# Optimization experiments

Hardware: AMD Instinct MI355X
Metric: run time of the kernel (lower is better)

The kernel has to match this reference:

```python
import math
import jax, jax.numpy as jnp
import numpy as np

NUM_EMBED = 2048
EMBED_FEATS = 64
IN_FEATS = 512
B, T = 16, 4096
COMMITMENT_COST = 0.25


def setup_inputs() -> dict:
    key = jax.random.key(0)
    k1, k2, k3, k4 = jax.random.split(key, 4)
    x = jax.random.normal(k1, (B, IN_FEATS, T), dtype=jnp.float32)
    proj_w = jax.random.normal(k2, (EMBED_FEATS, IN_FEATS), dtype=jnp.float32) / np.sqrt(IN_FEATS)
    proj_b = jax.random.normal(k3, (EMBED_FEATS,), dtype=jnp.float32) * 0.01
    embed = jax.random.normal(k4, (NUM_EMBED, EMBED_FEATS), dtype=jnp.float32)
    return {"x": x, "proj_w": proj_w, "proj_b": proj_b, "embed": embed}


def reference(x, proj_w, proj_b, embed):
    # 1x1 Conv1d projection, then transpose(1,-1): [B, Cin, T] -> [B, T, E]
    h = jnp.einsum('ec,bct->bte', proj_w, x) + proj_b  # [B, T, E]
    Bb, Tt, E = h.shape
    K = embed.shape[0]
    flat = h.reshape(-1, E)  # [N, E]
    # squared distances to codewords: [N, K]
    d2 = (jnp.sum(flat * flat, axis=1, keepdims=True)
          + jnp.sum(embed * embed, axis=1)
          - 2.0 * flat @ embed.T)
    q_idx = jnp.argmin(d2, axis=1)  # [N]
    z_q = embed[q_idx].reshape(Bb, Tt, E)  # one-hot @ embed == gather
    # commitment loss (codebook updated by EMA, so only commitment term)
    commitment = jnp.mean((jax.lax.stop_gradient(z_q) - h) ** 2)
    loss = COMMITMENT_COST * commitment
    # straight-through estimator
    z_q_st = h + jax.lax.stop_gradient(z_q - h)
    # code usage stats
    N = flat.shape[0]
    probs = jnp.zeros((K,), dtype=jnp.float32).at[q_idx].add(1.0) / N
    log_perplexity = -jnp.sum(probs * jnp.log(probs + 1e-10))
    kldiv_r = math.log(K) * (N / Bb) * jnp.ones((Bb, 1), dtype=jnp.float32)
    z_q_out = jnp.swapaxes(z_q_st, 1, 2)  # [B, E, T]
    return z_q_out, loss, kldiv_r, log_perplexity
```

## Files before the change

kernel.cpp:

```cpp
#include <hip/hip_runtime.h>
#include <math.h>

#define B_ 16
#define T_ 4096
#define C_ 512
#define E_ 64
#define K_ 2048
#define N_ (B_*T_)
#define ZQ_ELEMS 4194304

typedef __attribute__((ext_vector_type(8))) short short8;
typedef __attribute__((ext_vector_type(4))) short short4v;
typedef __attribute__((ext_vector_type(4))) float f32x4;

#define WS_EHI   0
#define WS_ELO   262144
#define WS_NHCC  524288
#define WS_WHI   532480
#define WS_WLO   598016
#define WS_HIST  663552
#define WS_LOSS  671744
#define WS_HIMG  1048576
#define WS_NEED  (WS_HIMG + 512*16384*2)

struct HiLo { short hi, lo; };

__device__ __forceinline__ unsigned short rne16(float v) {
    unsigned u = __float_as_uint(v);
    return (unsigned short)((u + 0x7FFFu + ((u >> 16) & 1u)) >> 16);
}
__device__ __forceinline__ HiLo split_rne(float v) {
    HiLo r;
    unsigned hb = rne16(v);
    r.hi = (short)hb;
    float hf = __uint_as_float((unsigned)hb << 16);
    r.lo = (short)rne16(v - hf);
    return r;
}

typedef const __attribute__((address_space(1))) void* gas1_t;
typedef __attribute__((address_space(3))) void* las3_t;
__device__ __forceinline__ void gl16(const void* g, void* l) {
    __builtin_amdgcn_global_load_lds((gas1_t)g, (las3_t)l, 16, 0, 0);
}

__global__ void prep_kernel(const float* __restrict__ embed,
                            const float* __restrict__ W,
                            short* __restrict__ ehi, short* __restrict__ elo,
                            float* __restrict__ nhcc,
                            short* __restrict__ whi, short* __restrict__ wlo) {
    const int tid = threadIdx.x;
    if (blockIdx.x < 64) {
        const int row = blockIdx.x * 32 + (tid >> 3);
        const int g = tid & 7;
        const float* src = embed + (size_t)row * 64 + g * 8;
        short8 hv, lv;
        float s = 0.f;
#pragma unroll
        for (int j = 0; j < 8; ++j) {
            float v = src[j];
            s = fmaf(v, v, s);
            HiLo r = split_rne(v);
            hv[j] = r.hi; lv[j] = r.lo;
        }
        const int c128 = row >> 7, r = row & 127;
        const int kt = r >> 4, col = r & 15, ks = g >> 2, qe = g & 3;
        const int slot = (kt * 2 + ks) * 64 + qe * 16 + col;
        *(short8*)(ehi + c128 * 8192 + slot * 8) = hv;
        *(short8*)(elo + c128 * 8192 + slot * 8) = lv;
        s += __shfl_xor(s, 1, 64);
        s += __shfl_xor(s, 2, 64);
        s += __shfl_xor(s, 4, 64);
        if (g == 0) nhcc[row] = -0.5f * s;
    } else {
        int idx = ((blockIdx.x - 64) * 256 + tid) * 4;
        float4 v = *(const float4*)(W + idx);
        short4v h, l;
        HiLo a = split_rne(v.x); h[0] = a.hi; l[0] = a.lo;
        HiLo b = split_rne(v.y); h[1] = b.hi; l[1] = b.lo;
        HiLo c = split_rne(v.z); h[2] = c.hi; l[2] = c.lo;
        HiLo d = split_rne(v.w); h[3] = d.hi; l[3] = d.lo;
        *(short4v*)(whi + idx) = h;
        *(short4v*)(wlo + idx) = l;
    }
}

__global__ __launch_bounds__(256, 2) void proj_kernel(
        const float* __restrict__ x,
        const short* __restrict__ whi, const short* __restrict__ wlo,
        const float* __restrict__ bias,
        short* __restrict__ himg, float* __restrict__ lossacc) {
    __shared__ __align__(16) float xw[4 * 32 * 66];

    const int tid = threadIdx.x;
    const int wave = tid >> 6, lane = tid & 63;
    const int row16 = lane & 15, quad = lane >> 4;
    const int blk = blockIdx.x;
    const int b  = blk >> 4;
    const int t0 = (blk & 15) * 256;
    const int t0w = t0 + wave * 64;
    const float* xr = x + (size_t)b * C_ * T_ + t0w;
    float* wl = xw + wave * (32 * 66);

    const int c_row = lane >> 4;
    const int c_t4  = (lane & 15) * 4;

    f32x4 acc[4][4];
#pragma unroll
    for (int rt = 0; rt < 4; ++rt)
#pragma unroll
        for (int et = 0; et < 4; ++et) acc[rt][et] = (f32x4){0.f, 0.f, 0.f, 0.f};

    float4 xn[8];
#pragma unroll
    for (int q = 0; q < 8; ++q)
        xn[q] = *(const float4*)(xr + (size_t)(q * 4 + c_row) * T_ + c_t4);

    for (int it = 0; it < 16; ++it) {
        const int c0 = it * 32;
#pragma unroll
        for (int q = 0; q < 8; ++q) {
            float* d = wl + (q * 4 + c_row) * 66 + c_t4;
            *(float2*)(d)     = make_float2(xn[q].x, xn[q].y);
            *(float2*)(d + 2) = make_float2(xn[q].z, xn[q].w);
        }
        if (it < 15) {
#pragma unroll
            for (int q = 0; q < 8; ++q)
                xn[q] = *(const float4*)(xr + (size_t)(c0 + 32 + q * 4 + c_row) * T_ + c_t4);
        }
#pragma unroll
        for (int rp = 0; rp < 2; ++rp) {
            short8 bh[2], bl[2];
#pragma unroll
            for (int rr = 0; rr < 2; ++rr) {
                const int rt = rp * 2 + rr;
#pragma unroll
                for (int j = 0; j < 8; ++j) {
                    float v = wl[(quad * 8 + j) * 66 + rt * 16 + row16];
                    HiLo r = split_rne(v);
                    bh[rr][j] = r.hi; bl[rr][j] = r.lo;
                }
            }
#pragma unroll
            for (int et = 0; et < 4; ++et) {
                size_t aoff = (size_t)(et * 16 + row16) * C_ + c0 + quad * 8;
                short8 ah = *(const short8*)(whi + aoff);
                short8 al = *(const short8*)(wlo + aoff);
#pragma unroll
                for (int rr = 0; rr < 2; ++rr) {
                    const int rt = rp * 2 + rr;
                    acc[rt][et] = __builtin_amdgcn_mfma_f32_16x16x32_bf16(ah, bh[rr], acc[rt][et], 0, 0, 0);
                    acc[rt][et] = __builtin_amdgcn_mfma_f32_16x16x32_bf16(al, bh[rr], acc[rt][et], 0, 0, 0);
                    acc[rt][et] = __builtin_amdgcn_mfma_f32_16x16x32_bf16(ah, bl[rr], acc[rt][et], 0, 0, 0);
                    acc[rt][et] = __builtin_amdgcn_mfma_f32_16x16x32_bf16(al, bl[rr], acc[rt][et], 0, 0, 0);
                }
            }
        }
    }

    float hh = 0.f;
#pragma unroll
    for (int rt = 0; rt < 4; ++rt) {
        const int tile16 = wave * 4 + rt;
        short* gb = himg + (size_t)(blk * 2 + (tile16 >> 3)) * 16384;
        const int w2 = tile16 & 7;
#pragma unroll
        for (int et = 0; et < 4; ++et) {
            float4 bv = *(const float4*)(bias + et * 16 + quad * 4);
            f32x4 a = acc[rt][et];
            a[0] += bv.x; a[1] += bv.y; a[2] += bv.z; a[3] += bv.w;
            hh = fmaf(a[0], a[0], hh); hh = fmaf(a[1], a[1], hh);
            hh = fmaf(a[2], a[2], hh); hh = fmaf(a[3], a[3], hh);
            short4v hv, lv;
#pragma unroll
            for (int r = 0; r < 4; ++r) {
                HiLo sp = split_rne(a[r]);
                hv[r] = sp.hi; lv[r] = sp.lo;
            }
            const int ks = et >> 1;
            const int qe = (et & 1) * 2 + (quad >> 1);
            const int j0 = (quad & 1) * 4;
            const int sl = ((w2 * 2 + ks) * 64 + qe * 16 + row16) * 8 + j0;
            *(short4v*)(gb + sl) = hv;
            *(short4v*)(gb + 8192 + sl) = lv;
        }
    }
#pragma unroll
    for (int m = 1; m < 64; m <<= 1) hh += __shfl_xor(hh, m, 64);
    if (lane == 0) atomicAdd(lossacc, hh);
}

#define VQ_STEP(H0, H1, L0, L1, SS)                                            \
    {                                                                          \
        const int kk = ((SS) >> 2) * 128 + (kh * 4 + ((SS) & 3)) * 16 + row16; \
        const float ci = nhcc[kk];                                             \
        _Pragma("unroll")                                                      \
        for (int rt = 0; rt < 4; ++rt) {                                       \
            f32x4 a2 = (f32x4){0.f, 0.f, 0.f, 0.f};                            \
            a2 = __builtin_amdgcn_mfma_f32_16x16x32_bf16(a_hi[rt][0], H0, a2, 0, 0, 0); \
            a2 = __builtin_amdgcn_mfma_f32_16x16x32_bf16(a_hi[rt][1], H1, a2, 0, 0, 0); \
            a2 = __builtin_amdgcn_mfma_f32_16x16x32_bf16(a_lo[rt][0], H0, a2, 0, 0, 0); \
            a2 = __builtin_amdgcn_mfma_f32_16x16x32_bf16(a_lo[rt][1], H1, a2, 0, 0, 0); \
            a2 = __builtin_amdgcn_mfma_f32_16x16x32_bf16(a_hi[rt][0], L0, a2, 0, 0, 0); \
            a2 = __builtin_amdgcn_mfma_f32_16x16x32_bf16(a_hi[rt][1], L1, a2, 0, 0, 0); \
            _Pragma("unroll")                                                  \
            for (int rg = 0; rg < 4; ++rg) {                                   \
                float v = a2[rg] + ci;                                         \
                if (v > vmax[rt][rg]) { vmax[rt][rg] = v; vidx[rt][rg] = kk; } \
            }                                                                  \
        }                                                                      \
    }

#define VQ_LOAD(H0, H1, L0, L1, SS)                                            \
    {                                                                          \
        const int c2 = (SS) >> 2, kt2 = kh * 4 + ((SS) & 3);                   \
        const short* pb = ehi + c2 * 8192 + kt2 * 1024;                        \
        const short* pl = elo + c2 * 8192 + kt2 * 1024;                        \
        H0 = *(const short8*)(pb + lane * 8);                                  \
        H1 = *(const short8*)(pb + 512 + lane * 8);                            \
        L0 = *(const short8*)(pl + lane * 8);                                  \
        L1 = *(const short8*)(pl + 512 + lane * 8);                            \
    }

__global__ __launch_bounds__(256, 2) void vq_kernel(
        const short* __restrict__ himg,
        const short* __restrict__ ehi, const short* __restrict__ elo,
        const float* __restrict__ nhcc,
        const float* __restrict__ embed, float* __restrict__ out,
        int* __restrict__ hist, float* __restrict__ lossacc) {
    __shared__ __align__(16) float tile[128 * 69];
    __shared__ int   qsm[128];
    __shared__ float vtmp[128];
    __shared__ int   itmp[128];

    const int tid = threadIdx.x;
    const int wave = tid >> 6, lane = tid & 63;
    const int row16 = lane & 15, quad = lane >> 4;
    const int g = blockIdx.x;
    const int b  = g >> 5;
    const int t0 = (g & 31) * 128;
    const int rowgrp = wave & 1, kh = wave >> 1;

    const short* gb = himg + (size_t)g * 16384;
    short8 a_hi[4][2], a_lo[4][2];
#pragma unroll
    for (int rt = 0; rt < 4; ++rt)
#pragma unroll
        for (int ks = 0; ks < 2; ++ks) {
            const int w2 = rowgrp * 4 + rt;
            const int sl = ((w2 * 2 + ks) * 64 + lane) * 8;
            a_hi[rt][ks] = *(const short8*)(gb + sl);
            a_lo[rt][ks] = *(const short8*)(gb + 8192 + sl);
        }

    float vmax[4][4];
    int   vidx[4][4];
#pragma unroll
    for (int rt = 0; rt < 4; ++rt)
#pragma unroll
        for (int rg = 0; rg < 4; ++rg) { vmax[rt][rg] = -3.4e38f; vidx[rt][rg] = 0; }

    short8 pAh0, pAh1, pAl0, pAl1;
    short8 pBh0, pBh1, pBl0, pBl1;
    VQ_LOAD(pAh0, pAh1, pAl0, pAl1, 0);
    for (int s = 0; s < 64; s += 2) {
        VQ_LOAD(pBh0, pBh1, pBl0, pBl1, s + 1);
        VQ_STEP(pAh0, pAh1, pAl0, pAl1, s);
        if (s + 2 < 64) VQ_LOAD(pAh0, pAh1, pAl0, pAl1, s + 2);
        VQ_STEP(pBh0, pBh1, pBl0, pBl1, s + 1);
    }

    float s_loss = 0.f;
#pragma unroll
    for (int rt = 0; rt < 4; ++rt)
#pragma unroll
        for (int rg = 0; rg < 4; ++rg) {
            float v = vmax[rt][rg];
            int ix = vidx[rt][rg];
#pragma unroll
            for (int m = 1; m < 16; m <<= 1) {
                float ov = __shfl_xor(v, m, 64);
                int   oi = __shfl_xor(ix, m, 64);
                if (ov > v || (ov == v && oi < ix)) { v = ov; ix = oi; }
            }
            vmax[rt][rg] = v; vidx[rt][rg] = ix;
        }
    if (kh == 1 && row16 == 0) {
#pragma unroll
        for (int rt = 0; rt < 4; ++rt)
#pragma unroll
            for (int rg = 0; rg < 4; ++rg) {
                const int row = (rowgrp * 4 + rt) * 16 + quad * 4 + rg;
                vtmp[row] = vmax[rt][rg];
                itmp[row] = vidx[rt][rg];
            }
    }
    __syncthreads();
    if (kh == 0) {
        if (row16 == 0) {
#pragma unroll
            for (int rt = 0; rt < 4; ++rt)
#pragma unroll
                for (int rg = 0; rg < 4; ++rg) {
                    const int row = (rowgrp * 4 + rt) * 16 + quad * 4 + rg;
                    float v = vmax[rt][rg];
                    int ix = vidx[rt][rg];
                    const float ov = vtmp[row];
                    const int   oi = itmp[row];
                    if (ov > v || (ov == v && oi < ix)) { v = ov; ix = oi; }
                    qsm[row] = ix;
                    atomicAdd(&hist[ix], 1);
                    s_loss += v;
                }
        }
        s_loss += __shfl_xor(s_loss, 16, 64);
        s_loss += __shfl_xor(s_loss, 32, 64);
        if (lane == 0) atomicAdd(lossacc, -2.f * s_loss);
    }
    __syncthreads();

    {
        const int r = tid >> 1, piece = tid & 1;
        const float* src = embed + (size_t)qsm[r] * 64 + piece * 32;
        float* dst = tile + r * 69 + piece * 32;
#pragma unroll
        for (int j = 0; j < 8; ++j)
            *(float4*)(dst + j * 4) = *(const float4*)(src + j * 4);
    }
    __syncthreads();
    {
        const int tt = tid & 63;
        const int eo = tid >> 6;
        float* ob = out + ((size_t)b * 64) * T_ + t0;
#pragma unroll
        for (int j = 0; j < 16; ++j) {
            const int e = j * 4 + eo;
            ob[(size_t)e * T_ + tt]      = tile[tt * 69 + e];
            ob[(size_t)e * T_ + 64 + tt] = tile[(tt + 64) * 69 + e];
        }
    }
}

__global__ __launch_bounds__(512, 4) void projvq_kernel(
        const float* __restrict__ x,
        const short* __restrict__ whi, const short* __restrict__ wlo,
        const float* __restrict__ bias,
        const short* __restrict__ ehi, const short* __restrict__ elo,
        const float* __restrict__ nhcc,
        const float* __restrict__ embed, float* __restrict__ out,
        int* __restrict__ hist, float* __restrict__ lossacc) {
    __shared__ __align__(16) char smem[68096];
    float* xsf  = (float*)smem;
    short* es   = (short*)smem;
    short* aimg = (short*)(smem + 32768);
    float* ccs  = (float*)(smem + 65536);
    int*   qsm2 = (int*)(smem + 66560);
    float* vtmp = (float*)(smem + 67072);
    int*   itmp = (int*)(smem + 67584);
    float* tile = (float*)smem;

    const int tid = threadIdx.x;
    const int wave = tid >> 6, lane = tid & 63;
    const int row16 = lane & 15, quad = lane >> 4;
    const int b  = blockIdx.x >> 5;
    const int t0 = (blockIdx.x & 31) * 128;
    const float* xb = x + (size_t)b * C_ * T_ + t0;

    f32x4 cc = *(const f32x4*)(nhcc + tid * 4);

    f32x4 acc[4];
#pragma unroll
    for (int et = 0; et < 4; ++et) acc[et] = (f32x4){0.f, 0.f, 0.f, 0.f};

#pragma unroll
    for (int j = 0; j < 2; ++j) {
        int o = j * 512 + tid;
        gl16(xb + (size_t)(o >> 5) * T_ + (o & 31) * 4, xsf + o * 4);
    }
    __syncthreads();

    for (int it = 0; it < 16; ++it) {
        const int c0 = it * 32;
        const int p = it & 1;
        if (it < 15) {
#pragma unroll
            for (int j = 0; j < 2; ++j) {
                int o = j * 512 + tid;
                gl16(xb + (size_t)(c0 + 32 + (o >> 5)) * T_ + (o & 31) * 4,
                     xsf + (p ^ 1) * 4096 + o * 4);
            }
        }
        const float* xsb = xsf + p * 4096;
        short8 bh, bl;
#pragma unroll
        for (int j = 0; j < 8; ++j) {
            float v = xsb[(quad * 8 + j) * 128 + wave * 16 + row16];
            HiLo r = split_rne(v);
            bh[j] = r.hi; bl[j] = r.lo;
        }
#pragma unroll
        for (int et = 0; et < 4; ++et) {
            size_t aoff = (size_t)(et * 16 + row16) * C_ + c0 + quad * 8;
            short8 ah = *(const short8*)(whi + aoff);
            short8 al = *(const short8*)(wlo + aoff);
            acc[et] = __builtin_amdgcn_mfma_f32_16x16x32_bf16(ah, bh, acc[et], 0, 0, 0);
            acc[et] = __builtin_amdgcn_mfma_f32_16x16x32_bf16(al, bh, acc[et], 0, 0, 0);
            acc[et] = __builtin_amdgcn_mfma_f32_16x16x32_bf16(ah, bl, acc[et], 0, 0, 0);
            acc[et] = __builtin_amdgcn_mfma_f32_16x16x32_bf16(al, bl, acc[et], 0, 0, 0);
        }
        __syncthreads();
    }

#pragma unroll
    for (int j = 0; j < 2; ++j) {
        int o = (j * 512 + tid) * 8;
        gl16(ehi + o, es + o);
        gl16(elo + o, es + 8192 + o);
    }

    float hh = 0.f;
#pragma unroll
    for (int et = 0; et < 4; ++et) {
        float4 bv = *(const float4*)(bias + et * 16 + quad * 4);
        f32x4 a = acc[et];
        a[0] += bv.x; a[1] += bv.y; a[2] += bv.z; a[3] += bv.w;
        hh = fmaf(a[0], a[0], hh); hh = fmaf(a[1], a[1], hh);
        hh = fmaf(a[2], a[2], hh); hh = fmaf(a[3], a[3], hh);
        short4v hv, lv;
#pragma unroll
        for (int r = 0; r < 4; ++r) {
            HiLo sp = split_rne(a[r]);
            hv[r] = sp.hi; lv[r] = sp.lo;
        }
        const int ks = et >> 1;
        const int qe = (et & 1) * 2 + (quad >> 1);
        const int j0 = (quad & 1) * 4;
        const int sl = ((wave * 2 + ks) * 64 + qe * 16 + row16) * 8 + j0;
        *(short4v*)(aimg + sl) = hv;
        *(short4v*)(aimg + 8192 + sl) = lv;
    }
#pragma unroll
    for (int m = 1; m < 64; m <<= 1) hh += __shfl_xor(hh, m, 64);
    if (lane == 0) atomicAdd(lossacc, hh);
    __syncthreads();

    const int pair = wave & 3, kh = wave >> 2;
    short8 a_hi[2][2], a_lo[2][2];
#pragma unroll
    for (int rt = 0; rt < 2; ++rt)
#pragma unroll
        for (int ks = 0; ks < 2; ++ks) {
            int sl = (((2 * pair + rt) * 2 + ks) * 64 + lane) * 8;
            a_hi[rt][ks] = *(const short8*)(aimg + sl);
            a_lo[rt][ks] = *(const short8*)(aimg + 8192 + sl);
        }
    if ((tid >> 5) == 0) *(f32x4*)(ccs + (tid & 31) * 4) = cc;
    __syncthreads();

    float vmax[2][4];
    int   vidx[2][4];
#pragma unroll
    for (int rt = 0; rt < 2; ++rt)
#pragma unroll
        for (int rg = 0; rg < 4; ++rg) { vmax[rt][rg] = -3.4e38f; vidx[rt][rg] = 0; }

    for (int c = 0; c < 16; ++c) {
        if (c < 15) {
            const short* sh  = ehi + (c + 1) * 8192;
            const short* sl2 = elo + (c + 1) * 8192;
            short* dst = es + ((c + 1) & 1) * 16384;
#pragma unroll
            for (int j = 0; j < 2; ++j) {
                int o = (j * 512 + tid) * 8;
                gl16(sh + o, dst + o);
                gl16(sl2 + o, dst + 8192 + o);
            }
            if ((tid >> 5) == c + 1)
                *(f32x4*)(ccs + ((c + 1) & 1) * 128 + (tid & 31) * 4) = cc;
        }
        const short* eb = es + (c & 1) * 16384;
        const float* cb = ccs + (c & 1) * 128;
#pragma unroll
        for (int k4 = 0; k4 < 4; ++k4) {
            const int kt = kh * 4 + k4;
            const float ci = cb[kt * 16 + row16];
            const short* pb = eb + kt * 1024;
            short8 bh0 = *(const short8*)(pb + lane * 8);
            short8 bh1 = *(const short8*)(pb + 512 + lane * 8);
            short8 bl0 = *(const short8*)(pb + 8192 + lane * 8);
            short8 bl1 = *(const short8*)(pb + 8192 + 512 + lane * 8);
            const int kk = c * 128 + kt * 16 + row16;
#pragma unroll
            for (int rt = 0; rt < 2; ++rt) {
                f32x4 a2 = (f32x4){0.f, 0.f, 0.f, 0.f};
                a2 = __builtin_amdgcn_mfma_f32_16x16x32_bf16(a_hi[rt][0], bh0, a2, 0, 0, 0);
                a2 = __builtin_amdgcn_mfma_f32_16x16x32_bf16(a_hi[rt][1], bh1, a2, 0, 0, 0);
                a2 = __builtin_amdgcn_mfma_f32_16x16x32_bf16(a_lo[rt][0], bh0, a2, 0, 0, 0);
                a2 = __builtin_amdgcn_mfma_f32_16x16x32_bf16(a_lo[rt][1], bh1, a2, 0, 0, 0);
                a2 = __builtin_amdgcn_mfma_f32_16x16x32_bf16(a_hi[rt][0], bl0, a2, 0, 0, 0);
                a2 = __builtin_amdgcn_mfma_f32_16x16x32_bf16(a_hi[rt][1], bl1, a2, 0, 0, 0);
#pragma unroll
                for (int rg = 0; rg < 4; ++rg) {
                    float v = a2[rg] + ci;
                    if (v > vmax[rt][rg]) { vmax[rt][rg] = v; vidx[rt][rg] = kk; }
                }
            }
        }
        __syncthreads();
    }

    float s = 0.f;
#pragma unroll
    for (int rt = 0; rt < 2; ++rt)
#pragma unroll
        for (int rg = 0; rg < 4; ++rg) {
            float v = vmax[rt][rg];
            int ix = vidx[rt][rg];
#pragma unroll
            for (int m = 1; m < 16; m <<= 1) {
                float ov = __shfl_xor(v, m, 64);
                int   oi = __shfl_xor(ix, m, 64);
                if (ov > v || (ov == v && oi < ix)) { v = ov; ix = oi; }
            }
            vmax[rt][rg] = v; vidx[rt][rg] = ix;
        }
    if (kh == 1 && row16 == 0) {
#pragma unroll
        for (int rt = 0; rt < 2; ++rt)
#pragma unroll
            for (int rg = 0; rg < 4; ++rg) {
                const int row = (2 * pair + rt) * 16 + quad * 4 + rg;
                vtmp[row] = vmax[rt][rg];
                itmp[row] = vidx[rt][rg];
            }
    }
    __syncthreads();
    if (kh == 0) {
        if (row16 == 0) {
#pragma unroll
            for (int rt = 0; rt < 2; ++rt)
#pragma unroll
                for (int rg = 0; rg < 4; ++rg) {
                    const int row = (2 * pair + rt) * 16 + quad * 4 + rg;
                    float v = vmax[rt][rg];
                    int ix = vidx[rt][rg];
                    const float ov = vtmp[row];
                    const int   oi = itmp[row];
                    if (ov > v || (ov == v && oi < ix)) { v = ov; ix = oi; }
                    qsm2[row] = ix;
                    atomicAdd(&hist[ix], 1);
                    s += v;
                }
        }
        s += __shfl_xor(s, 16, 64);
        s += __shfl_xor(s, 32, 64);
        if (lane == 0) atomicAdd(lossacc, -2.f * s);
    }
    __syncthreads();

    {
        const int r = tid >> 2, piece = tid & 3;
        const float* src = embed + (size_t)qsm2[r] * 64 + piece * 16;
        float* dst = tile + r * 69 + piece * 16;
#pragma unroll
        for (int j = 0; j < 4; ++j)
            *(float4*)(dst + j * 4) = *(const float4*)(src + j * 4);
    }
    __syncthreads();
    {
        const int tt = tid & 63;
        const int eo = tid >> 6;
#pragma unroll
        for (int j = 0; j < 8; ++j) {
            const int e = j * 8 + eo;
            float* ob = out + ((size_t)b * 64) * T_ + t0;
            ob[(size_t)e * T_ + tt]      = tile[tt * 69 + e];
            ob[(size_t)e * T_ + 64 + tt] = tile[(tt + 64) * 69 + e];
        }
    }
}

__global__ void finalize_kernel(const int* __restrict__ hist,
                                const float* __restrict__ lossacc,
                                float* __restrict__ out) {
    __shared__ float red[4];
    const int tid = threadIdx.x;
    float s = 0.f;
    for (int k = tid; k < K_; k += 256) {
        float p = (float)hist[k] * (1.f / 65536.f);
        s -= p * logf(p + 1e-10f);
    }
#pragma unroll
    for (int m = 1; m < 64; m <<= 1) s += __shfl_xor(s, m, 64);
    if ((tid & 63) == 0) red[tid >> 6] = s;
    __syncthreads();
    if (tid == 0) {
        float lp = red[0] + red[1] + red[2] + red[3];
        out[ZQ_ELEMS] = 0.25f * lossacc[0] / (float)ZQ_ELEMS;
        out[ZQ_ELEMS + 17] = lp;
    }
    if (tid < 16) out[ZQ_ELEMS + 1 + tid] = logf(2048.f) * 4096.f;
}

extern "C" void kernel_launch(void* const* d_in, const int* in_sizes, int n_in,
                              void* d_out, int out_size, void* d_ws, size_t ws_size,
                              hipStream_t stream) {
    const float* x      = (const float*)d_in[0];
    const float* proj_w = (const float*)d_in[1];
    const float* proj_b = (const float*)d_in[2];
    const float* embed  = (const float*)d_in[3];
    float* out = (float*)d_out;
    char* ws = (char*)d_ws;

    short* e_hi = (short*)(ws + WS_EHI);
    short* e_lo = (short*)(ws + WS_ELO);
    float* nhcc = (float*)(ws + WS_NHCC);
    short* w_hi = (short*)(ws + WS_WHI);
    short* w_lo = (short*)(ws + WS_WLO);
    int*   hist = (int*)(ws + WS_HIST);
    float* lossac = (float*)(ws + WS_LOSS);
    short* himg = (short*)(ws + WS_HIMG);

    (void)hipMemsetAsync(ws + WS_HIST, 0, K_ * sizeof(int) + sizeof(float), stream);

    prep_kernel<<<96, 256, 0, stream>>>(embed, proj_w, e_hi, e_lo, nhcc, w_hi, w_lo);
    if (ws_size >= (size_t)WS_NEED) {
        proj_kernel<<<256, 256, 0, stream>>>(x, w_hi, w_lo, proj_b, himg, lossac);
        vq_kernel<<<512, 256, 0, stream>>>(himg, e_hi, e_lo, nhcc, embed, out,
                                           hist, lossac);
    } else {
        projvq_kernel<<<N_ / 128, 512, 0, stream>>>(x, w_hi, w_lo, proj_b,
                                                    e_hi, e_lo, nhcc, embed, out,
                                                    hist, lossac);
    }
    finalize_kernel<<<1, 256, 0, stream>>>(hist, lossac, out);
}
```

Baseline: 299.9 us.

## Split projection over channels and VQ codebook over more waves per block

The projection kernel now uses 512 blocks of 128 timesteps, with wave pairs splitting the 512 input channels in half and reducing partial accumulators through shared memory. The VQ kernel doubles to 512 threads so four wave groups each scan a quarter of the codebook, merging per-row argmax candidates from three partner groups in shared memory. Both changes aim to raise parallelism and occupancy on a grid that otherwise underfills the GPU. In exchange they add extra LDS traffic and synchronisation, and larger VQ blocks may increase register pressure.

```diff
diff --git a/kernel.cpp b/kernel.cpp
--- a/kernel.cpp
+++ b/kernel.cpp
@@ -91,19 +91,21 @@
         const float* __restrict__ bias,
         short* __restrict__ himg, float* __restrict__ lossacc) {
     __shared__ __align__(16) float xw[4 * 32 * 66];
-
     const int tid = threadIdx.x;
     const int wave = tid >> 6, lane = tid & 63;
     const int row16 = lane & 15, quad = lane >> 4;
     const int blk = blockIdx.x;
-    const int b  = blk >> 4;
-    const int t0 = (blk & 15) * 256;
-    const int t0w = t0 + wave * 64;
+    const int b  = blk >> 5;
+    const int t0 = (blk & 31) * 128;
+    const int tl = wave & 1;
+    const int cs = wave >> 1;
+    const int t0w = t0 + tl * 64;
     const float* xr = x + (size_t)b * C_ * T_ + t0w;
     float* wl = xw + wave * (32 * 66);
 
     const int c_row = lane >> 4;
     const int c_t4  = (lane & 15) * 4;
+    const int cbase = cs * 256;
 
     f32x4 acc[4][4];
 #pragma unroll
@@ -114,17 +116,17 @@
     float4 xn[8];
 #pragma unroll
     for (int q = 0; q < 8; ++q)
-        xn[q] = *(const float4*)(xr + (size_t)(q * 4 + c_row) * T_ + c_t4);
-
-    for (int it = 0; it < 16; ++it) {
-        const int c0 = it * 32;
+        xn[q] = *(const float4*)(xr + (size_t)(cbase + q * 4 + c_row) * T_ + c_t4);
+
+    for (int it = 0; it < 8; ++it) {
+        const int c0 = cbase + it * 32;
 #pragma unroll
         for (int q = 0; q < 8; ++q) {
             float* d = wl + (q * 4 + c_row) * 66 + c_t4;
             *(float2*)(d)     = make_float2(xn[q].x, xn[q].y);
             *(float2*)(d + 2) = make_float2(xn[q].z, xn[q].w);
         }
-        if (it < 15) {
+        if (it < 7) {
 #pragma unroll
             for (int q = 0; q < 8; ++q)
                 xn[q] = *(const float4*)(xr + (size_t)(c0 + 32 + q * 4 + c_row) * T_ + c_t4);
@@ -159,41 +161,63 @@
         }
     }
 
-    float hh = 0.f;
-#pragma unroll
-    for (int rt = 0; rt < 4; ++rt) {
-        const int tile16 = wave * 4 + rt;
-        short* gb = himg + (size_t)(blk * 2 + (tile16 >> 3)) * 16384;
-        const int w2 = tile16 & 7;
-#pragma unroll
-        for (int et = 0; et < 4; ++et) {
-            float4 bv = *(const float4*)(bias + et * 16 + quad * 4);
-            f32x4 a = acc[rt][et];
-            a[0] += bv.x; a[1] += bv.y; a[2] += bv.z; a[3] += bv.w;
-            hh = fmaf(a[0], a[0], hh); hh = fmaf(a[1], a[1], hh);
-            hh = fmaf(a[2], a[2], hh); hh = fmaf(a[3], a[3], hh);
-            short4v hv, lv;
-#pragma unroll
-            for (int r = 0; r < 4; ++r) {
-                HiLo sp = split_rne(a[r]);
-                hv[r] = sp.hi; lv[r] = sp.lo;
-            }
-            const int ks = et >> 1;
-            const int qe = (et & 1) * 2 + (quad >> 1);
-            const int j0 = (quad & 1) * 4;
-            const int sl = ((w2 * 2 + ks) * 64 + qe * 16 + row16) * 8 + j0;
-            *(short4v*)(gb + sl) = hv;
-            *(short4v*)(gb + 8192 + sl) = lv;
-        }
-    }
-#pragma unroll
-    for (int m = 1; m < 64; m <<= 1) hh += __shfl_xor(hh, m, 64);
-    if (lane == 0) atomicAdd(lossacc, hh);
+    __syncthreads();
+    if (cs == 1) {
+#pragma unroll
+        for (int rt = 0; rt < 4; ++rt)
+#pragma unroll
+            for (int et = 0; et < 4; ++et)
+#pragma unroll
+                for (int r = 0; r < 4; ++r)
+                    xw[(tl * 64 + et * 16 + quad * 4 + r) * 66 + rt * 16 + row16] =
+                        acc[rt][et][r];
+    }
+    __syncthreads();
+    if (cs == 0) {
+#pragma unroll
+        for (int rt = 0; rt < 4; ++rt)
+#pragma unroll
+            for (int et = 0; et < 4; ++et)
+#pragma unroll
+                for (int r = 0; r < 4; ++r)
+                    acc[rt][et][r] +=
+                        xw[(tl * 64 + et * 16 + quad * 4 + r) * 66 + rt * 16 + row16];
+
+        short* gb = himg + (size_t)blk * 16384;
+        float hh = 0.f;
+#pragma unroll
+        for (int rt = 0; rt < 4; ++rt) {
+            const int w2 = tl * 4 + rt;
+#pragma unroll
+            for (int et = 0; et < 4; ++et) {
+                float4 bv = *(const float4*)(bias + et * 16 + quad * 4);
+                f32x4 a = acc[rt][et];
+                a[0] += bv.x; a[1] += bv.y; a[2] += bv.z; a[3] += bv.w;
+                hh = fmaf(a[0], a[0], hh); hh = fmaf(a[1], a[1], hh);
+                hh = fmaf(a[2], a[2], hh); hh = fmaf(a[3], a[3], hh);
+                short4v hv, lv;
+#pragma unroll
+                for (int r = 0; r < 4; ++r) {
+                    HiLo sp = split_rne(a[r]);
+                    hv[r] = sp.hi; lv[r] = sp.lo;
+                }
+                const int ks = et >> 1;
+                const int qe = (et & 1) * 2 + (quad >> 1);
+                const int j0 = (quad & 1) * 4;
+                const int sl = ((w2 * 2 + ks) * 64 + qe * 16 + row16) * 8 + j0;
+                *(short4v*)(gb + sl) = hv;
+                *(short4v*)(gb + 8192 + sl) = lv;
+            }
+        }
+#pragma unroll
+        for (int m = 1; m < 64; m <<= 1) hh += __shfl_xor(hh, m, 64);
+        if (lane == 0) atomicAdd(lossacc, hh);
+    }
 }
 
 #define VQ_STEP(H0, H1, L0, L1, SS)                                            \
     {                                                                          \
-        const int kk = ((SS) >> 2) * 128 + (kh * 4 + ((SS) & 3)) * 16 + row16; \
+        const int kk = ((SS) >> 1) * 128 + (kh * 2 + ((SS) & 1)) * 16 + row16; \
         const float ci = nhcc[kk];                                             \
         _Pragma("unroll")                                                      \
         for (int rt = 0; rt < 4; ++rt) {                                       \
@@ -214,7 +238,7 @@
 
 #define VQ_LOAD(H0, H1, L0, L1, SS)                                            \
     {                                                                          \
-        const int c2 = (SS) >> 2, kt2 = kh * 4 + ((SS) & 3);                   \
+        const int c2 = (SS) >> 1, kt2 = kh * 2 + ((SS) & 1);                   \
         const short* pb = ehi + c2 * 8192 + kt2 * 1024;                        \
         const short* pl = elo + c2 * 8192 + kt2 * 1024;                        \
         H0 = *(const short8*)(pb + lane * 8);                                  \
@@ -223,7 +247,7 @@
         L1 = *(const short8*)(pl + 512 + lane * 8);                            \
     }
 
-__global__ __launch_bounds__(256, 2) void vq_kernel(
+__global__ __launch_bounds__(512, 4) void vq_kernel(
         const short* __restrict__ himg,
         const short* __restrict__ ehi, const short* __restrict__ elo,
         const float* __restrict__ nhcc,
@@ -231,8 +255,8 @@
         int* __restrict__ hist, float* __restrict__ lossacc) {
     __shared__ __align__(16) float tile[128 * 69];
     __shared__ int   qsm[128];
-    __shared__ float vtmp[128];
-    __shared__ int   itmp[128];
+    __shared__ float vtmp[3 * 128];
+    __shared__ int   itmp[3 * 128];
 
     const int tid = threadIdx.x;
     const int wave = tid >> 6, lane = tid & 63;
@@ -264,10 +288,10 @@
     short8 pAh0, pAh1, pAl0, pAl1;
     short8 pBh0, pBh1, pBl0, pBl1;
     VQ_LOAD(pAh0, pAh1, pAl0, pAl1, 0);
-    for (int s = 0; s < 64; s += 2) {
+    for (int s = 0; s < 32; s += 2) {
         VQ_LOAD(pBh0, pBh1, pBl0, pBl1, s + 1);
         VQ_STEP(pAh0, pAh1, pAl0, pAl1, s);
-        if (s + 2 < 64) VQ_LOAD(pAh0, pAh1, pAl0, pAl1, s + 2);
+        if (s + 2 < 32) VQ_LOAD(pAh0, pAh1, pAl0, pAl1, s + 2);
         VQ_STEP(pBh0, pBh1, pBl0, pBl1, s + 1);
     }
 
@@ -286,14 +310,14 @@
             }
             vmax[rt][rg] = v; vidx[rt][rg] = ix;
         }
-    if (kh == 1 && row16 == 0) {
+    if (kh >= 1 && row16 == 0) {
 #pragma unroll
         for (int rt = 0; rt < 4; ++rt)
 #pragma unroll
             for (int rg = 0; rg < 4; ++rg) {
                 const int row = (rowgrp * 4 + rt) * 16 + quad * 4 + rg;
-                vtmp[row] = vmax[rt][rg];
-                itmp[row] = vidx[rt][rg];
+                vtmp[(kh - 1) * 128 + row] = vmax[rt][rg];
+                itmp[(kh - 1) * 128 + row] = vidx[rt][rg];
             }
     }
     __syncthreads();
@@ -306,9 +330,12 @@
                     const int row = (rowgrp * 4 + rt) * 16 + quad * 4 + rg;
                     float v = vmax[rt][rg];
                     int ix = vidx[rt][rg];
-                    const float ov = vtmp[row];
-                    const int   oi = itmp[row];
-                    if (ov > v || (ov == v && oi < ix)) { v = ov; ix = oi; }
+#pragma unroll
+                    for (int p = 0; p < 3; ++p) {
+                        const float ov = vtmp[p * 128 + row];
+                        const int   oi = itmp[p * 128 + row];
+                        if (ov > v || (ov == v && oi < ix)) { v = ov; ix = oi; }
+                    }
                     qsm[row] = ix;
                     atomicAdd(&hist[ix], 1);
                     s_loss += v;
@@ -321,11 +348,11 @@
     __syncthreads();
 
     {
-        const int r = tid >> 1, piece = tid & 1;
-        const float* src = embed + (size_t)qsm[r] * 64 + piece * 32;
-        float* dst = tile + r * 69 + piece * 32;
-#pragma unroll
-        for (int j = 0; j < 8; ++j)
+        const int r = tid >> 2, piece = tid & 3;
+        const float* src = embed + (size_t)qsm[r] * 64 + piece * 16;
+        float* dst = tile + r * 69 + piece * 16;
+#pragma unroll
+        for (int j = 0; j < 4; ++j)
             *(float4*)(dst + j * 4) = *(const float4*)(src + j * 4);
     }
     __syncthreads();
@@ -334,8 +361,8 @@
         const int eo = tid >> 6;
         float* ob = out + ((size_t)b * 64) * T_ + t0;
 #pragma unroll
-        for (int j = 0; j < 16; ++j) {
-            const int e = j * 4 + eo;
+        for (int j = 0; j < 8; ++j) {
+            const int e = j * 8 + eo;
             ob[(size_t)e * T_ + tt]      = tile[tt * 69 + e];
             ob[(size_t)e * T_ + 64 + tt] = tile[(tt + 64) * 69 + e];
         }
@@ -626,8 +653,8 @@
 
     prep_kernel<<<96, 256, 0, stream>>>(embed, proj_w, e_hi, e_lo, nhcc, w_hi, w_lo);
     if (ws_size >= (size_t)WS_NEED) {
-        proj_kernel<<<256, 256, 0, stream>>>(x, w_hi, w_lo, proj_b, himg, lossac);
-        vq_kernel<<<512, 256, 0, stream>>>(himg, e_hi, e_lo, nhcc, embed, out,
+        proj_kernel<<<512, 256, 0, stream>>>(x, w_hi, w_lo, proj_b, himg, lossac);
+        vq_kernel<<<512, 512, 0, stream>>>(himg, e_hi, e_lo, nhcc, embed, out,
                                            hist, lossac);
     } else {
         projvq_kernel<<<N_ / 128, 512, 0, stream>>>(x, w_hi, w_lo, proj_b,
```

New measurement: 453.3 us. +51.1%, slower.
